# Optimization experiments

Measured on AMD Instinct MI355X. Metric: run time of the kernel, lower is better.

The kernel has to match this reference:

```python
import jax, jax.numpy as jnp
import numpy as np

CUTOFF = 5.0
N_ENV = 8
F0, F1 = 16, 32  # filter_dims
D = 256          # feature_dim


def setup_inputs() -> dict:
    key = jax.random.key(0)
    ks = jax.random.split(key, 12)
    B, E, N = 128, 64, 32
    r = jax.random.normal(ks[0], (B, E, 3), jnp.float32) * 3.0
    # neighbors placed near r so distances fall inside the cutoff
    r_nb = r[..., None, :] + jax.random.normal(ks[1], (B, E, N, 3), jnp.float32) * 1.5
    ee_scales = jax.random.uniform(ks[2], (N_ENV,), jnp.float32, 0.5, CUTOFF)
    ee_kernel = jax.random.normal(ks[3], (4, F0), jnp.float32) / jnp.sqrt(4.0)
    ee_bias = jax.random.normal(ks[4], (F0,), jnp.float32) * 2.0
    beta_kernel = jax.random.normal(ks[5], (F0 + N_ENV, F1), jnp.float32) / jnp.sqrt(F0 + N_ENV + 0.0)
    beta_bias = jnp.zeros((F1,), jnp.float32)
    gamma_kernel = jax.random.normal(ks[6], (F1, D), jnp.float32) / jnp.sqrt(F1 + 0.0)
    dense1_kernel = jax.random.normal(ks[7], (4, D), jnp.float32) / jnp.sqrt(4.0)
    dense1_bias = jnp.zeros((D,), jnp.float32)
    out_kernel = jax.random.normal(ks[8], (D, D), jnp.float32) / jnp.sqrt(D + 0.0)
    out_bias = jnp.zeros((D,), jnp.float32)
    return dict(r=r, r_nb=r_nb, ee_scales=ee_scales, ee_kernel=ee_kernel, ee_bias=ee_bias,
                beta_kernel=beta_kernel, beta_bias=beta_bias, gamma_kernel=gamma_kernel,
                dense1_kernel=dense1_kernel, dense1_bias=dense1_bias,
                out_kernel=out_kernel, out_bias=out_bias)


def reference(r, r_nb, ee_scales, ee_kernel, ee_bias, beta_kernel, beta_bias,
              gamma_kernel, dense1_kernel, dense1_bias, out_kernel, out_bias):
    # pairwise diff features: [dist, dx, dy, dz] per neighbor
    diff = r_nb - r[..., None, :]                       # [B,E,N,3]
    dist = jnp.linalg.norm(diff, axis=-1, keepdims=True)  # [B,E,N,1]
    feats = jnp.concatenate([dist, diff], axis=-1)      # [B,E,N,4]

    # PairwiseFilter (beta_ee): envelopes + small dense, gated by smooth cutoff
    env = jnp.exp(-jnp.square(dist / ee_scales))        # [B,E,N,N_ENV]
    h = jnp.tanh(feats @ ee_kernel + ee_bias)           # [B,E,N,F0]
    x = dist / CUTOFF
    fcut = jnp.where(x < 1.0, 0.5 * (jnp.cos(jnp.pi * x) + 1.0), 0.0)
    beta = (jnp.concatenate([h, env], axis=-1) @ beta_kernel + beta_bias) * fcut  # [B,E,N,F1]

    gamma = beta @ gamma_kernel                         # [B,E,N,D]

    # rescale features: first column (dist) becomes log1p(dist)
    inp = feats / dist * jnp.log1p(dist)                # [B,E,N,4]
    feat = jax.nn.silu(inp @ dense1_kernel + dense1_bias)  # [B,E,N,D]

    res = jnp.einsum('...id,...id->...d', feat, gamma)  # sum over neighbors -> [B,E,D]
    res = jax.nn.silu(res @ out_kernel + out_bias)
    return res
```

## Files before the change

kernel.cpp:

```cpp
#include <hip/hip_runtime.h>
#include <hip/hip_bf16.h>

constexpr int NB   = 32;
constexpr int NENV = 8;
constexpr int F0   = 16;
constexpr int F1   = 32;
constexpr int D    = 256;
constexpr int PAIRS = 128 * 64;
constexpr float CUT = 5.0f;
constexpr int WT_STRIDE = 264;

typedef float f32x4 __attribute__((ext_vector_type(4)));
typedef short s16x8 __attribute__((ext_vector_type(8)));

__device__ __forceinline__ float fast_rcp(float x) { return __builtin_amdgcn_rcpf(x); }
__device__ __forceinline__ float silu(float a) {
  return a * fast_rcp(1.0f + __expf(-a));
}
__device__ __forceinline__ float fast_tanh(float t) {
  return 1.0f - 2.0f * fast_rcp(__expf(2.0f * t) + 1.0f);
}
__device__ __forceinline__ unsigned short f2bf(float f) {
  __hip_bfloat16 h = __float2bfloat16(f);
  unsigned short u; __builtin_memcpy(&u, &h, 2); return u;
}

__global__ __launch_bounds__(256) void moon_prep(
    const float* __restrict__ out_kernel,
    unsigned short* __restrict__ wt)
{
  const int i  = blockIdx.x * 256 + threadIdx.x;
  const int d  = i >> 6;
  const int kg = i & 63;
  ushort4 p;
  p.x = f2bf(out_kernel[(4 * kg + 0) * D + d]);
  p.y = f2bf(out_kernel[(4 * kg + 1) * D + d]);
  p.z = f2bf(out_kernel[(4 * kg + 2) * D + d]);
  p.w = f2bf(out_kernel[(4 * kg + 3) * D + d]);
  *(ushort4*)&wt[d * WT_STRIDE + 4 * kg] = p;
}

__global__ __launch_bounds__(256)
__attribute__((amdgpu_waves_per_eu(4, 4)))
void moon_fused(
    const float* __restrict__ r,
    const float* __restrict__ r_nb,
    const float* __restrict__ ee_scales,
    const float* __restrict__ ee_kernel,
    const float* __restrict__ ee_bias,
    const float* __restrict__ beta_kernel,
    const float* __restrict__ beta_bias,
    const float* __restrict__ gamma_kernel,
    const float* __restrict__ dense1_kernel,
    const float* __restrict__ dense1_bias,
    const unsigned short* __restrict__ wt,
    const float* __restrict__ out_bias,
    float* __restrict__ out)
{
  __shared__ float s_eek[4 * F0];
  __shared__ float s_eeb[F0];
  __shared__ float s_bk[(F0 + NENV) * F1];
  __shared__ float s_bb[F1];
  __shared__ float s_is2[NENV];
  __shared__ unsigned short s_ghT[4][D * 8];
  __shared__ unsigned short s_d1kT[D * 8];
  __shared__ unsigned short s_betah[4][4][NB * 8];
  __shared__ unsigned short s_inph[4][NB * 8];
  __shared__ unsigned short s_resall[4 * 264];

  const int tid = threadIdx.x;
  const int w   = tid >> 6;
  const int l   = tid & 63;
  const int be  = blockIdx.x * 4 + w;
  const int be0 = blockIdx.x * 4;

  for (int i = tid; i < 888; i += 256) {
    if (i < 64)        s_eek[i]       = ee_kernel[i];
    else if (i < 80)   s_eeb[i - 64]  = ee_bias[i - 64];
    else if (i < 848)  s_bk[i - 80]   = beta_kernel[i - 80];
    else if (i < 880)  s_bb[i - 848]  = beta_bias[i - 848];
    else { float s = ee_scales[i - 880]; s_is2[i - 880] = 1.0f / (s * s); }
  }
  {
    const int d = tid;
    unsigned int pk[16];
    #pragma unroll
    for (int k2 = 0; k2 < 16; ++k2) {
      unsigned short lo = f2bf(gamma_kernel[(2 * k2 + 0) * D + d]);
      unsigned short hi = f2bf(gamma_kernel[(2 * k2 + 1) * D + d]);
      pk[k2] = (unsigned int)lo | ((unsigned int)hi << 16);
    }
    #pragma unroll
    for (int g = 0; g < 4; ++g)
      *(uint4*)&s_ghT[g][d * 8] = make_uint4(pk[4*g], pk[4*g+1], pk[4*g+2], pk[4*g+3]);
  }
  {
    const int d = tid;
    unsigned int p0 = (unsigned int)f2bf(0.25f * dense1_kernel[0 * D + d])
                    | ((unsigned int)f2bf(0.25f * dense1_kernel[1 * D + d]) << 16);
    unsigned int p1 = (unsigned int)f2bf(0.25f * dense1_kernel[2 * D + d])
                    | ((unsigned int)f2bf(0.25f * dense1_kernel[3 * D + d]) << 16);
    unsigned int p2 = (unsigned int)f2bf(0.25f * dense1_bias[d]);
    *(uint4*)&s_d1kT[d * 8] = make_uint4(p0, p1, p2, 0u);
  }

  __syncthreads();

  {
    const int n  = l & 31;
    const int cg = l >> 5;
    float rx = r[be * 3 + 0];
    float ry = r[be * 3 + 1];
    float rz = r[be * 3 + 2];
    const float* rn = r_nb + (be * NB + n) * 3;
    float dx = rn[0] - rx;
    float dy = rn[1] - ry;
    float dz = rn[2] - rz;
    float d2 = dx * dx + dy * dy + dz * dz;
    float dist = sqrtf(d2);
    float feats[4] = {dist, dx, dy, dz};
    float h[F0];
    #pragma unroll
    for (int j = 0; j < F0; ++j) {
      float t = s_eeb[j];
      #pragma unroll
      for (int i = 0; i < 4; ++i) t += feats[i] * s_eek[i * F0 + j];
      h[j] = fast_tanh(t);
    }
    float env[NENV];
    #pragma unroll
    for (int s = 0; s < NENV; ++s) env[s] = __expf(-d2 * s_is2[s]);
    float xc = dist * (1.0f / CUT);
    float fcut = (xc < 1.0f)
               ? 0.5f * (__cosf(3.14159265358979323846f * xc) + 1.0f)
               : 0.0f;
    if (cg == 0) {
      float lp = log1pf(dist);
      float inv = lp / dist;
      unsigned int q0 = (unsigned int)f2bf(lp) | ((unsigned int)f2bf(dx * inv) << 16);
      unsigned int q1 = (unsigned int)f2bf(dy * inv) | ((unsigned int)f2bf(dz * inv) << 16);
      *(uint4*)&s_inph[w][n * 8] = make_uint4(q0, q1, 0x3F80u , 0u);
    }
    unsigned int pk[8];
    #pragma unroll
    for (int c4 = 0; c4 < 4; ++c4) {
      float bb[4];
      #pragma unroll
      for (int cc = 0; cc < 4; ++cc) {
        int c = cg * 16 + c4 * 4 + cc;
        float a = s_bb[c];
        #pragma unroll
        for (int k = 0; k < F0; ++k) a += h[k] * s_bk[k * F1 + c];
        #pragma unroll
        for (int s = 0; s < NENV; ++s) a += env[s] * s_bk[(F0 + s) * F1 + c];
        bb[cc] = a * fcut;
      }
      pk[c4 * 2 + 0] = (unsigned int)f2bf(bb[0]) | ((unsigned int)f2bf(bb[1]) << 16);
      pk[c4 * 2 + 1] = (unsigned int)f2bf(bb[2]) | ((unsigned int)f2bf(bb[3]) << 16);
    }
    *(uint4*)&s_betah[w][2 * cg + 0][n * 8] = make_uint4(pk[0], pk[1], pk[2], pk[3]);
    *(uint4*)&s_betah[w][2 * cg + 1][n * 8] = make_uint4(pk[4], pk[5], pk[6], pk[7]);
  }
  __syncthreads();

  const int li = l & 15;
  const int g  = l >> 4;

  s16x8 a0 = *(const s16x8*)&s_betah[w][g][(0 * 16 + li) * 8];
  s16x8 a1 = *(const s16x8*)&s_betah[w][g][(1 * 16 + li) * 8];
  s16x8 ai0 = *(const s16x8*)&s_inph[w][(0 * 16 + li) * 8];
  s16x8 ai1 = *(const s16x8*)&s_inph[w][(1 * 16 + li) * 8];

  #pragma unroll 4
  for (int nt = 0; nt < 16; ++nt) {
    const int d = nt * 16 + li;
    s16x8 b  = *(const s16x8*)&s_ghT[g][d * 8];
    s16x8 bd = *(const s16x8*)&s_d1kT[d * 8];
    f32x4 z = {0.f, 0.f, 0.f, 0.f};
    f32x4 c0 = __builtin_amdgcn_mfma_f32_16x16x32_bf16(a0, b, z, 0, 0, 0);
    f32x4 c1 = __builtin_amdgcn_mfma_f32_16x16x32_bf16(a1, b, z, 0, 0, 0);
    f32x4 f0 = __builtin_amdgcn_mfma_f32_16x16x32_bf16(ai0, bd, z, 0, 0, 0);
    f32x4 f1 = __builtin_amdgcn_mfma_f32_16x16x32_bf16(ai1, bd, z, 0, 0, 0);
    float p = 0.f;
    #pragma unroll
    for (int reg = 0; reg < 4; ++reg) {
      p += silu(f0[reg]) * c0[reg];
      p += silu(f1[reg]) * c1[reg];
    }
    p += __shfl_xor(p, 16);
    p += __shfl_xor(p, 32);
    if (g == (nt & 3)) s_resall[w * 264 + nt * 16 + li] = f2bf(p);
  }
  __syncthreads();

  {
    const int col0 = w * 64;
    float bi[4];
    #pragma unroll
    for (int nt = 0; nt < 4; ++nt) bi[nt] = out_bias[col0 + nt * 16 + li];

    f32x4 acc[4] = {{0.f,0.f,0.f,0.f},{0.f,0.f,0.f,0.f},{0.f,0.f,0.f,0.f},{0.f,0.f,0.f,0.f}};
    const unsigned short* arow = &s_resall[(li & 3) * 264 + g * 8];
    const unsigned short* bp   = wt + (col0 + li) * WT_STRIDE + g * 8;

    #pragma unroll
    for (int ks = 0; ks < 8; ++ks) {
      s16x8 a = *(const s16x8*)(arow + ks * 32);
      #pragma unroll
      for (int nt = 0; nt < 4; ++nt) {
        s16x8 b = *(const s16x8*)(bp + nt * 16 * WT_STRIDE + ks * 32);
        acc[nt] = __builtin_amdgcn_mfma_f32_16x16x32_bf16(a, b, acc[nt], 0, 0, 0);
      }
    }
    if (g == 0) {
      #pragma unroll
      for (int nt = 0; nt < 4; ++nt) {
        #pragma unroll
        for (int reg = 0; reg < 4; ++reg) {
          out[(be0 + reg) * D + col0 + nt * 16 + li] = silu(acc[nt][reg] + bi[nt]);
        }
      }
    }
  }
}

extern "C" void kernel_launch(void* const* d_in, const int* in_sizes, int n_in,
                              void* d_out, int out_size, void* d_ws, size_t ws_size,
                              hipStream_t stream) {
  const float* r            = (const float*)d_in[0];
  const float* r_nb         = (const float*)d_in[1];
  const float* ee_scales    = (const float*)d_in[2];
  const float* ee_kernel    = (const float*)d_in[3];
  const float* ee_bias      = (const float*)d_in[4];
  const float* beta_kernel  = (const float*)d_in[5];
  const float* beta_bias    = (const float*)d_in[6];
  const float* gamma_kernel = (const float*)d_in[7];
  const float* dense1_kernel= (const float*)d_in[8];
  const float* dense1_bias  = (const float*)d_in[9];
  const float* out_kernel   = (const float*)d_in[10];
  const float* out_bias     = (const float*)d_in[11];
  float* out = (float*)d_out;

  unsigned short* wt = (unsigned short*)d_ws;

  hipLaunchKernelGGL(moon_prep, dim3(64), dim3(256), 0, stream, out_kernel, wt);
  hipLaunchKernelGGL(moon_fused, dim3(PAIRS / 4), dim3(256), 0, stream,
                     r, r_nb, ee_scales, ee_kernel, ee_bias,
                     beta_kernel, beta_bias, gamma_kernel,
                     dense1_kernel, dense1_bias, wt, out_bias, out);
}
```

Baseline: 124.2 us.

## Compute beta filter with bf16 MFMA and split envelope work across half-waves

Replaces the per-lane scalar FMA loop for the beta dense layer (24x32 weights, done twice per neighbour) with four bf16 16x16x32 MFMAs on packed h/env/bias operands. The cutoff factor is applied afterwards, and the result is written back in place into the same LDS buffer. The tanh, envelope and fcut work is now split between the two half-waves instead of being duplicated, and conversions use the packed v_cvt_pk_bf16_f32 instruction. The block barrier between the filter and the gamma stage is dropped because all data stays wave-local. In exchange, the beta weights, h and the envelopes are rounded to bf16, and correctness relies on in-order LDS access within a wave.

```diff
diff --git a/kernel.cpp b/kernel.cpp
--- a/kernel.cpp
+++ b/kernel.cpp
@@ -20,9 +20,13 @@
 __device__ __forceinline__ float fast_tanh(float t) {
   return 1.0f - 2.0f * fast_rcp(__expf(2.0f * t) + 1.0f);
 }
+__device__ __forceinline__ unsigned int cvt_pk_bf16(float a, float b) {
+  unsigned int r;
+  asm("v_cvt_pk_bf16_f32 %0, %1, %2" : "=v"(r) : "v"(a), "v"(b));
+  return r;
+}
 __device__ __forceinline__ unsigned short f2bf(float f) {
-  __hip_bfloat16 h = __float2bfloat16(f);
-  unsigned short u; __builtin_memcpy(&u, &h, 2); return u;
+  return (unsigned short)(cvt_pk_bf16(f, f) & 0xffffu);
 }
 
 __global__ __launch_bounds__(256) void moon_prep(
@@ -32,12 +36,11 @@
   const int i  = blockIdx.x * 256 + threadIdx.x;
   const int d  = i >> 6;
   const int kg = i & 63;
-  ushort4 p;
-  p.x = f2bf(out_kernel[(4 * kg + 0) * D + d]);
-  p.y = f2bf(out_kernel[(4 * kg + 1) * D + d]);
-  p.z = f2bf(out_kernel[(4 * kg + 2) * D + d]);
-  p.w = f2bf(out_kernel[(4 * kg + 3) * D + d]);
-  *(ushort4*)&wt[d * WT_STRIDE + 4 * kg] = p;
+  unsigned int p0 = cvt_pk_bf16(out_kernel[(4 * kg + 0) * D + d],
+                                out_kernel[(4 * kg + 1) * D + d]);
+  unsigned int p1 = cvt_pk_bf16(out_kernel[(4 * kg + 2) * D + d],
+                                out_kernel[(4 * kg + 3) * D + d]);
+  *(uint2*)&wt[d * WT_STRIDE + 4 * kg] = make_uint2(p0, p1);
 }
 
 __global__ __launch_bounds__(256)
@@ -59,13 +62,13 @@
 {
   __shared__ float s_eek[4 * F0];
   __shared__ float s_eeb[F0];
-  __shared__ float s_bk[(F0 + NENV) * F1];
-  __shared__ float s_bb[F1];
   __shared__ float s_is2[NENV];
   __shared__ unsigned short s_ghT[4][D * 8];
   __shared__ unsigned short s_d1kT[D * 8];
-  __shared__ unsigned short s_betah[4][4][NB * 8];
+  __shared__ unsigned short s_bkh[4][F1 * 8];
+  __shared__ unsigned short s_hb[4][4][NB * 8];
   __shared__ unsigned short s_inph[4][NB * 8];
+  __shared__ float s_fcut[4][NB];
   __shared__ unsigned short s_resall[4 * 264];
 
   const int tid = threadIdx.x;
@@ -74,41 +77,55 @@
   const int be  = blockIdx.x * 4 + w;
   const int be0 = blockIdx.x * 4;
 
-  for (int i = tid; i < 888; i += 256) {
-    if (i < 64)        s_eek[i]       = ee_kernel[i];
-    else if (i < 80)   s_eeb[i - 64]  = ee_bias[i - 64];
-    else if (i < 848)  s_bk[i - 80]   = beta_kernel[i - 80];
-    else if (i < 880)  s_bb[i - 848]  = beta_bias[i - 848];
-    else { float s = ee_scales[i - 880]; s_is2[i - 880] = 1.0f / (s * s); }
-  }
+  if (tid < 64)       s_eek[tid]      = ee_kernel[tid];
+  else if (tid < 80)  s_eeb[tid - 64] = ee_bias[tid - 64];
+  else if (tid < 88) { float s = ee_scales[tid - 80]; s_is2[tid - 80] = 1.0f / (s * s); }
+
+  if (tid < 128) {
+    const int c = tid & 31;
+    const int g = tid >> 5;
+    unsigned int q[4];
+    if (g < 3) {
+      float v[8];
+      #pragma unroll
+      for (int j = 0; j < 8; ++j) v[j] = beta_kernel[(g * 8 + j) * F1 + c];
+      q[0] = cvt_pk_bf16(v[0], v[1]); q[1] = cvt_pk_bf16(v[2], v[3]);
+      q[2] = cvt_pk_bf16(v[4], v[5]); q[3] = cvt_pk_bf16(v[6], v[7]);
+    } else {
+      q[0] = cvt_pk_bf16(beta_bias[c], 0.0f); q[1] = 0; q[2] = 0; q[3] = 0;
+    }
+    *(uint4*)&s_bkh[g][c * 8] = make_uint4(q[0], q[1], q[2], q[3]);
+  }
+
   {
     const int d = tid;
     unsigned int pk[16];
     #pragma unroll
-    for (int k2 = 0; k2 < 16; ++k2) {
-      unsigned short lo = f2bf(gamma_kernel[(2 * k2 + 0) * D + d]);
-      unsigned short hi = f2bf(gamma_kernel[(2 * k2 + 1) * D + d]);
-      pk[k2] = (unsigned int)lo | ((unsigned int)hi << 16);
-    }
+    for (int k2 = 0; k2 < 16; ++k2)
+      pk[k2] = cvt_pk_bf16(gamma_kernel[(2 * k2 + 0) * D + d],
+                           gamma_kernel[(2 * k2 + 1) * D + d]);
     #pragma unroll
     for (int g = 0; g < 4; ++g)
       *(uint4*)&s_ghT[g][d * 8] = make_uint4(pk[4*g], pk[4*g+1], pk[4*g+2], pk[4*g+3]);
   }
   {
     const int d = tid;
-    unsigned int p0 = (unsigned int)f2bf(0.25f * dense1_kernel[0 * D + d])
-                    | ((unsigned int)f2bf(0.25f * dense1_kernel[1 * D + d]) << 16);
-    unsigned int p1 = (unsigned int)f2bf(0.25f * dense1_kernel[2 * D + d])
-                    | ((unsigned int)f2bf(0.25f * dense1_kernel[3 * D + d]) << 16);
-    unsigned int p2 = (unsigned int)f2bf(0.25f * dense1_bias[d]);
+    unsigned int p0 = cvt_pk_bf16(0.25f * dense1_kernel[0 * D + d],
+                                  0.25f * dense1_kernel[1 * D + d]);
+    unsigned int p1 = cvt_pk_bf16(0.25f * dense1_kernel[2 * D + d],
+                                  0.25f * dense1_kernel[3 * D + d]);
+    unsigned int p2 = cvt_pk_bf16(0.25f * dense1_bias[d], 0.0f);
     *(uint4*)&s_d1kT[d * 8] = make_uint4(p0, p1, p2, 0u);
   }
 
   __syncthreads();
 
-  {
-    const int n  = l & 31;
-    const int cg = l >> 5;
+  const int li = l & 15;
+  const int g  = l >> 4;
+
+  {
+    const int n    = l & 31;
+    const int half = l >> 5;
     float rx = r[be * 3 + 0];
     float ry = r[be * 3 + 1];
     float rz = r[be * 3 + 2];
@@ -119,55 +136,71 @@
     float d2 = dx * dx + dy * dy + dz * dz;
     float dist = sqrtf(d2);
     float feats[4] = {dist, dx, dy, dz};
-    float h[F0];
-    #pragma unroll
-    for (int j = 0; j < F0; ++j) {
+    float h[8];
+    #pragma unroll
+    for (int j8 = 0; j8 < 8; ++j8) {
+      int j = half * 8 + j8;
       float t = s_eeb[j];
       #pragma unroll
       for (int i = 0; i < 4; ++i) t += feats[i] * s_eek[i * F0 + j];
-      h[j] = fast_tanh(t);
-    }
-    float env[NENV];
-    #pragma unroll
-    for (int s = 0; s < NENV; ++s) env[s] = __expf(-d2 * s_is2[s]);
-    float xc = dist * (1.0f / CUT);
-    float fcut = (xc < 1.0f)
-               ? 0.5f * (__cosf(3.14159265358979323846f * xc) + 1.0f)
-               : 0.0f;
-    if (cg == 0) {
-      float lp = log1pf(dist);
+      h[j8] = fast_tanh(t);
+    }
+    unsigned int hp0 = cvt_pk_bf16(h[0], h[1]);
+    unsigned int hp1 = cvt_pk_bf16(h[2], h[3]);
+    unsigned int hp2 = cvt_pk_bf16(h[4], h[5]);
+    unsigned int hp3 = cvt_pk_bf16(h[6], h[7]);
+    if (half == 0) {
+      *(uint4*)&s_hb[w][0][n * 8] = make_uint4(hp0, hp1, hp2, hp3);
+      *(uint4*)&s_hb[w][3][n * 8] = make_uint4(0x3F80u, 0u, 0u, 0u);
+      float lp  = log1pf(dist);
       float inv = lp / dist;
-      unsigned int q0 = (unsigned int)f2bf(lp) | ((unsigned int)f2bf(dx * inv) << 16);
-      unsigned int q1 = (unsigned int)f2bf(dy * inv) | ((unsigned int)f2bf(dz * inv) << 16);
-      *(uint4*)&s_inph[w][n * 8] = make_uint4(q0, q1, 0x3F80u , 0u);
-    }
-    unsigned int pk[8];
-    #pragma unroll
-    for (int c4 = 0; c4 < 4; ++c4) {
-      float bb[4];
-      #pragma unroll
-      for (int cc = 0; cc < 4; ++cc) {
-        int c = cg * 16 + c4 * 4 + cc;
-        float a = s_bb[c];
-        #pragma unroll
-        for (int k = 0; k < F0; ++k) a += h[k] * s_bk[k * F1 + c];
-        #pragma unroll
-        for (int s = 0; s < NENV; ++s) a += env[s] * s_bk[(F0 + s) * F1 + c];
-        bb[cc] = a * fcut;
-      }
-      pk[c4 * 2 + 0] = (unsigned int)f2bf(bb[0]) | ((unsigned int)f2bf(bb[1]) << 16);
-      pk[c4 * 2 + 1] = (unsigned int)f2bf(bb[2]) | ((unsigned int)f2bf(bb[3]) << 16);
-    }
-    *(uint4*)&s_betah[w][2 * cg + 0][n * 8] = make_uint4(pk[0], pk[1], pk[2], pk[3]);
-    *(uint4*)&s_betah[w][2 * cg + 1][n * 8] = make_uint4(pk[4], pk[5], pk[6], pk[7]);
-  }
-  __syncthreads();
-
-  const int li = l & 15;
-  const int g  = l >> 4;
-
-  s16x8 a0 = *(const s16x8*)&s_betah[w][g][(0 * 16 + li) * 8];
-  s16x8 a1 = *(const s16x8*)&s_betah[w][g][(1 * 16 + li) * 8];
+      unsigned int q0 = cvt_pk_bf16(lp, dx * inv);
+      unsigned int q1 = cvt_pk_bf16(dy * inv, dz * inv);
+      *(uint4*)&s_inph[w][n * 8] = make_uint4(q0, q1, 0x3F80u, 0u);
+    } else {
+      *(uint4*)&s_hb[w][1][n * 8] = make_uint4(hp0, hp1, hp2, hp3);
+      float env[NENV];
+      #pragma unroll
+      for (int s = 0; s < NENV; ++s) env[s] = __expf(-d2 * s_is2[s]);
+      unsigned int e0 = cvt_pk_bf16(env[0], env[1]);
+      unsigned int e1 = cvt_pk_bf16(env[2], env[3]);
+      unsigned int e2 = cvt_pk_bf16(env[4], env[5]);
+      unsigned int e3 = cvt_pk_bf16(env[6], env[7]);
+      *(uint4*)&s_hb[w][2][n * 8] = make_uint4(e0, e1, e2, e3);
+      float xc = dist * (1.0f / CUT);
+      s_fcut[w][n] = (xc < 1.0f)
+                   ? 0.5f * (__cosf(3.14159265358979323846f * xc) + 1.0f)
+                   : 0.0f;
+    }
+  }
+
+  {
+    s16x8 ah0 = *(const s16x8*)&s_hb[w][g][(0 * 16 + li) * 8];
+    s16x8 ah1 = *(const s16x8*)&s_hb[w][g][(1 * 16 + li) * 8];
+    s16x8 bb0 = *(const s16x8*)&s_bkh[g][(0 * 16 + li) * 8];
+    s16x8 bb1 = *(const s16x8*)&s_bkh[g][(1 * 16 + li) * 8];
+    f32x4 z = {0.f, 0.f, 0.f, 0.f};
+    f32x4 c00 = __builtin_amdgcn_mfma_f32_16x16x32_bf16(ah0, bb0, z, 0, 0, 0);
+    f32x4 c01 = __builtin_amdgcn_mfma_f32_16x16x32_bf16(ah0, bb1, z, 0, 0, 0);
+    f32x4 c10 = __builtin_amdgcn_mfma_f32_16x16x32_bf16(ah1, bb0, z, 0, 0, 0);
+    f32x4 c11 = __builtin_amdgcn_mfma_f32_16x16x32_bf16(ah1, bb1, z, 0, 0, 0);
+    const int cl = li >> 3;
+    const int sl = li & 7;
+    #pragma unroll
+    for (int reg = 0; reg < 4; ++reg) {
+      int row0 = g * 4 + reg;
+      int row1 = 16 + g * 4 + reg;
+      float fc0 = s_fcut[w][row0];
+      float fc1 = s_fcut[w][row1];
+      s_hb[w][cl    ][row0 * 8 + sl] = f2bf(c00[reg] * fc0);
+      s_hb[w][2 + cl][row0 * 8 + sl] = f2bf(c01[reg] * fc0);
+      s_hb[w][cl    ][row1 * 8 + sl] = f2bf(c10[reg] * fc1);
+      s_hb[w][2 + cl][row1 * 8 + sl] = f2bf(c11[reg] * fc1);
+    }
+  }
+
+  s16x8 a0 = *(const s16x8*)&s_hb[w][g][(0 * 16 + li) * 8];
+  s16x8 a1 = *(const s16x8*)&s_hb[w][g][(1 * 16 + li) * 8];
   s16x8 ai0 = *(const s16x8*)&s_inph[w][(0 * 16 + li) * 8];
   s16x8 ai1 = *(const s16x8*)&s_inph[w][(1 * 16 + li) * 8];
 
```

Result: faster. 117.3 us (-5.6%).
